# Optimization experiments

Measured on AMD Instinct MI355X. Metric: run time of the kernel, lower is better.

## Reference

```python
import jax, jax.numpy as jnp
import numpy as np
import math

B, S, D_MODEL, HEADS, HK = 1024, 81, 64, 4, 16  # S=81 from dim1=5184/64; HK=head dim
FFN, LAYERS, NCLS = 128, 2, 16
EPS = 1e-5


def setup_inputs() -> dict:
    key = jax.random.key(0)
    ks = iter(jax.random.split(key, 40))
    def rn(shape, scale=1.0):
        return jax.random.normal(next(ks), shape, jnp.float32) * scale
    d = {}
    d['X'] = rn((B, 1, 30, 13, 13))
    d['c3w'] = rn((8, 1, 3, 3, 3), 0.1); d['c3b'] = jnp.zeros((8,), jnp.float32)
    d['bn3g'] = jnp.ones((8,), jnp.float32); d['bn3b'] = jnp.zeros((8,), jnp.float32)
    d['c2w'] = rn((64, 224, 3, 3), 0.05); d['c2b'] = jnp.zeros((64,), jnp.float32)
    d['bn2g'] = jnp.ones((64,), jnp.float32); d['bn2b'] = jnp.zeros((64,), jnp.float32)
    d['wq'] = rn((LAYERS, HEADS, D_MODEL, HK), 1.0 / D_MODEL)
    d['wk'] = rn((LAYERS, HEADS, D_MODEL, HK), 1.0 / D_MODEL)
    d['wv'] = rn((LAYERS, HEADS, D_MODEL, HK), 1.0 / D_MODEL)
    d['wg'] = rn((LAYERS, D_MODEL, D_MODEL), 1.0 / D_MODEL)
    d['wo'] = rn((LAYERS, D_MODEL, D_MODEL), 1.0 / D_MODEL)
    d['gng'] = jnp.ones((LAYERS, D_MODEL), jnp.float32); d['gnb'] = jnp.zeros((LAYERS, D_MODEL), jnp.float32)
    d['ln1g'] = jnp.ones((LAYERS, D_MODEL), jnp.float32); d['ln1b'] = jnp.zeros((LAYERS, D_MODEL), jnp.float32)
    d['ln2g'] = jnp.ones((LAYERS, D_MODEL), jnp.float32); d['ln2b'] = jnp.zeros((LAYERS, D_MODEL), jnp.float32)
    d['fw1'] = rn((LAYERS, D_MODEL, FFN), 0.05); d['fb1'] = jnp.zeros((LAYERS, FFN), jnp.float32)
    d['fw2'] = rn((LAYERS, FFN, D_MODEL), 0.05); d['fb2'] = jnp.zeros((LAYERS, D_MODEL), jnp.float32)
    d['nn1w'] = rn((S * D_MODEL, NCLS), 0.02); d['nn1b'] = rn((NCLS,), 1e-6)
    return d


def _bn(x, g, b, axes):
    # BatchNorm in training mode (module default): batch statistics, biased var
    mu = x.mean(axes, keepdims=True)
    var = x.var(axes, keepdims=True)
    shp = [1] * x.ndim; shp[1] = -1
    return (x - mu) / jnp.sqrt(var + EPS) * g.reshape(shp) + b.reshape(shp)


def _ln(x, g, b):
    mu = x.mean(-1, keepdims=True)
    var = x.var(-1, keepdims=True)
    return (x - mu) / jnp.sqrt(var + EPS) * g + b


def _rot2(x):
    # rotate_every_two: (x0,x1,x2,x3,...) -> (-x1,x0,-x3,x2,...)
    x1, x2 = x[..., ::2], x[..., 1::2]
    return jnp.stack((-x2, x1), axis=-1).reshape(x.shape)


def _xpos_tables():
    scale = (jnp.arange(0, HK, 2, dtype=jnp.float32) + 0.4 * HK) / (1.4 * HK)  # (HK/2,)
    pos = jnp.arange(S, dtype=jnp.float32)
    xs = scale[None, :] ** (pos[:, None] / 512.0)                               # (S, HK/2)
    inv_freq = 1.0 / (10000.0 ** (jnp.arange(HK // 2, dtype=jnp.float32) / (HK // 2)))
    ang = pos[:, None] * inv_freq[None, :]
    sin, cos = jnp.sin(ang), jnp.cos(ang)
    dup = lambda m: jnp.repeat(m, 2, axis=-1)                                   # (S, HK)
    return dup(cos * xs), dup(sin * xs), dup(cos / xs), dup(sin / xs)


def _decay_mask():
    g = 1.0 - jnp.exp(jnp.linspace(math.log(1 / 32), math.log(1 / 512), HEADS))
    nm = jnp.arange(S)[:, None] - jnp.arange(S)[None, :]
    return jnp.where(nm >= 0, g[:, None, None] ** nm, 0.0)                      # (H,S,S)


def _forward(X, c3w, c3b, bn3g, bn3b, c2w, c2b, bn2g, bn2b,
             wq, wk, wv, wg, wo, gng, gnb, ln1g, ln1b, ln2g, ln2b,
             fw1, fb1, fw2, fb2, nn1w, nn1b):
    # Convnet front-end
    x = jax.lax.conv_general_dilated(X, c3w, (1, 1, 1), 'VALID',
                                     dimension_numbers=('NCDHW', 'OIDHW', 'NCDHW'))
    x = x + c3b[None, :, None, None, None]
    x = jax.nn.relu(_bn(x, bn3g, bn3b, (0, 2, 3, 4)))        # (B,8,28,11,11)
    x = x.reshape(B, 8 * 28, 11, 11)                           # 'b c h w y -> b (c h) w y'
    x = jax.lax.conv_general_dilated(x, c2w, (1, 1), 'VALID',
                                     dimension_numbers=('NCHW', 'OIHW', 'NCHW'))
    x = x + c2b[None, :, None, None]
    x = jax.nn.relu(_bn(x, bn2g, bn2b, (0, 2, 3)))           # (B,64,9,9)
    x = x.transpose(0, 2, 3, 1).reshape(B, S, D_MODEL)        # 'b c h w -> b (h w) c'

    cu, su, cd, sd = _xpos_tables()
    Dm = _decay_mask()
    for l in range(LAYERS):
        h = _ln(x, ln1g[l], ln1b[l])
        # per-head retention (parallel form)
        Q = jnp.einsum('bsd,hdk->bhsk', h, wq[l])
        K = jnp.einsum('bsd,hdk->bhsk', h, wk[l])
        V = jnp.einsum('bsd,hdk->bhsk', h, wv[l])
        Q = Q * cu + _rot2(Q) * su                            # xpos upscale
        K = K * cd + _rot2(K) * sd                            # xpos downscale
        att = jnp.einsum('bhsk,bhtk->bhst', Q, K) * Dm[None]  # decay-masked scores
        Yh = jnp.einsum('bhst,bhtv->bhsv', att, V)            # (B,H,S,HK)
        # GroupNorm(heads, v_dim) on (B*S, v_dim): per-(b,s,head) normalization
        mu = Yh.mean(-1, keepdims=True)
        var = Yh.var(-1, keepdims=True)
        Yh = (Yh - mu) / jnp.sqrt(var + EPS)
        Yc = Yh.transpose(0, 2, 1, 3).reshape(B, S, D_MODEL) * gng[l] + gnb[l]
        G = h @ wg[l]
        y = (G * jax.nn.sigmoid(G) * Yc) @ wo[l] + x          # swish gate + residual
        h2 = _ln(y, ln2g[l], ln2b[l])
        x = jax.nn.gelu(h2 @ fw1[l] + fb1[l], approximate=False) @ fw2[l] + fb2[l] + y
    return x.reshape(B, S * D_MODEL) @ nn1w + nn1b            # (B, NCLS)


def reference(X, c3w, c3b, bn3g, bn3b, c2w, c2b, bn2g, bn2b,
              wq, wk, wv, wg, wo, gng, gnb, ln1g, ln1b, ln2g, ln2b,
              fw1, fb1, fw2, fb2, nn1w, nn1b):
    return _forward(X, c3w, c3b, bn3g, bn3b, c2w, c2b, bn2g, bn2b,
                    wq, wk, wv, wg, wo, gng, gnb, ln1g, ln1b, ln2g, ln2b,
                    fw1, fb1, fw2, fb2, nn1w, nn1b)
```

## Files before the change

### kernel.cpp

```cpp
#include <hip/hip_runtime.h>
#include <math.h>

#define EPS 1e-5f

#define OFF_A  0u
#define OFF_X0 0u
#define OFF_Y  31850496u
#define OFF_CP 31850496u
#define OFF_WC 32374784u
#define OFF_B  47775744u
#define OFF_P  53084160u
#define OFF_RT 53084160u
#define OFF_ST 53215232u

#define WB_QKV 0u
#define WB_WG  24576u
#define WB_WO  32768u
#define WB_FW1 40960u
#define WB_FW2 57344u

typedef __attribute__((ext_vector_type(8))) short short8;
typedef __attribute__((ext_vector_type(4))) float f32x4;

__device__ inline unsigned short f2bf(float f) {
  unsigned int x = __float_as_uint(f);
  unsigned int r = x + 0x7fffu + ((x >> 16) & 1u);
  return (unsigned short)(r >> 16);
}
__device__ inline float bf2f(unsigned short h) {
  return __uint_as_float(((unsigned int)h) << 16);
}

__global__ __launch_bounds__(256) void kd1_conv1(const float* X, const float* c3w,
                                                 const float* c3b, float* ws) {
  __shared__ float Xi[5070];
  __shared__ float w3[216];
  int tid = threadIdx.x, b = blockIdx.x;
  for (int u = tid; u < 5070; u += 256) Xi[u] = X[(size_t)b*5070 + u];
  if (tid < 216) w3[tid] = c3w[tid];
  __syncthreads();
  if (tid >= 224) return;
  int o1 = tid / 28, dd = tid - o1*28;
  float wr[27];
#pragma unroll
  for (int k = 0; k < 27; ++k) wr[k] = w3[o1*27 + k];
  float bias = c3b[o1];
  unsigned short* Ao = (unsigned short*)(ws + OFF_A) + (size_t)b*27104;
  float S = 0.f, Q = 0.f;
  for (int h = 0; h < 11; ++h) {
    const float* base = Xi + dd*169 + h*13;
    float c0[9], c1[9], c2[9];
#pragma unroll
    for (int j = 0; j < 9; ++j) {
      int kd = j / 3, kh = j - kd*3;
      const float* rp = base + kd*169 + kh*13;
      c0[j] = rp[0]; c1[j] = rp[1]; c2[j] = rp[2];
    }
#pragma unroll
    for (int w = 0; w < 11; ++w) {
      float a = bias;
#pragma unroll
      for (int j = 0; j < 9; ++j) {
        a = fmaf(c0[j], wr[j*3+0], a);
        a = fmaf(c1[j], wr[j*3+1], a);
        a = fmaf(c2[j], wr[j*3+2], a);
      }
      Ao[(h*11 + w)*224 + tid] = f2bf(a);
      S += a; Q += a*a;
      if (w < 10) {
#pragma unroll
        for (int j = 0; j < 9; ++j) {
          int kd = j / 3, kh = j - kd*3;
          c0[j] = c1[j]; c1[j] = c2[j];
          c2[j] = base[kd*169 + kh*13 + w + 3];
        }
      }
    }
  }
  ws[OFF_CP + b*448 + tid]       = S;
  ws[OFF_CP + b*448 + 224 + tid] = Q;
}

__global__ void kd3_bn1fin(const float* ws_in, float* ws,
                           const float* bn3g, const float* bn3b) {
  __shared__ float sS[256], sQ[256];
  int t = threadIdx.x;
  int o1 = t >> 5, j = t & 31;
  float S = 0.f, Q = 0.f;
  for (int b = j; b < 1024; b += 32) {
    const float* P = ws_in + OFF_CP + b*448 + o1*28;
    for (int dd = 0; dd < 28; ++dd) { S += P[dd]; Q += P[224 + dd]; }
  }
  sS[t] = S; sQ[t] = Q;
  __syncthreads();
  if (j == 0) {
    float Ss = 0.f, Qs = 0.f;
    for (int k = 0; k < 32; ++k) { Ss += sS[o1*32 + k]; Qs += sQ[o1*32 + k]; }
    float n = 3469312.f;
    float mean = Ss / n;
    float var = Qs / n - mean*mean;
    float sc = bn3g[o1] * rsqrtf(var + EPS);
    ws[OFF_ST + o1]     = sc;
    ws[OFF_ST + 8 + o1] = bn3b[o1] - mean*sc;
  }
}

__global__ void k0wc(const float* c2w, float* ws) {
  int i = blockIdx.x*256 + threadIdx.x;
  if (i >= 129024) return;
  int ci = i % 224; int r = i / 224; int kpos = r % 9; int oc = r / 9;
  ((unsigned short*)(ws + OFF_WC))[i] = f2bf(c2w[oc*2016 + ci*9 + kpos]);
}

__global__ __launch_bounds__(256) void kd5_conv2_mfma(const float* ws_in, const float* c2b,
                                                      float* ws) {
  __shared__ unsigned short InT[121*232];
  __shared__ float bn1s[224], bn1sh[224];
  const int tid  = threadIdx.x;
  const int b    = blockIdx.x;
  const int wid  = tid >> 6;
  const int lane = tid & 63;
  const int lane15 = lane & 15;
  const int kgrp   = lane >> 4;
  if (tid < 224) {
    int o1 = tid / 28;
    bn1s[tid]  = ws_in[OFF_ST + o1];
    bn1sh[tid] = ws_in[OFF_ST + 8 + o1];
  }
  __syncthreads();
  const unsigned short* Ab = (const unsigned short*)(ws_in + OFF_A) + (size_t)b*27104;
  for (int e = tid; e < 27104; e += 256) {
    int pos = e / 224, ci = e - pos*224;
    float v = fmaxf(bn1s[ci]*bf2f(Ab[e]) + bn1sh[ci], 0.f);
    InT[pos*232 + ci] = f2bf(v);
  }
  __syncthreads();

  int r0[6];
#pragma unroll
  for (int mt = 0; mt < 6; ++mt) {
    int s = mt*16 + lane15; if (s > 80) s = 80;
    int y = s / 9;
    r0[mt] = y*11 + (s - y*9);
  }
  const unsigned short* wcb = (const unsigned short*)(ws_in + OFF_WC);
  const int col = wid*16 + lane15;
  f32x4 acc[6];
#pragma unroll
  for (int mt = 0; mt < 6; ++mt) acc[mt] = (f32x4){0.f,0.f,0.f,0.f};

  for (int kpos = 0; kpos < 9; ++kpos) {
    int ki = kpos / 3, kj = kpos - ki*3;
    int roff = ki*11 + kj;
    const unsigned short* wcp = wcb + ((size_t)col*9 + kpos)*224 + kgrp*8;
#pragma unroll
    for (int Ks = 0; Ks < 7; ++Ks) {
      short8 bf = *(const short8*)(wcp + Ks*32);
#pragma unroll
      for (int mt = 0; mt < 6; ++mt) {
        short8 af = *(const short8*)(InT + (r0[mt] + roff)*232 + Ks*32 + kgrp*8);
        acc[mt] = __builtin_amdgcn_mfma_f32_16x16x32_bf16(af, bf, acc[mt], 0, 0, 0);
      }
    }
  }
  float bias = c2b[col];
  float* Bb = ws + OFF_B + (size_t)b*5184 + col*81;
  float S = 0.f, Q = 0.f;
#pragma unroll
  for (int mt = 0; mt < 6; ++mt) {
#pragma unroll
    for (int r = 0; r < 4; ++r) {
      int s = mt*16 + kgrp*4 + r;
      if (s < 81) {
        float v = acc[mt][r] + bias;
        Bb[s] = v;
        S += v; Q += v*v;
      }
    }
  }
  S += __shfl_xor(S, 16); S += __shfl_xor(S, 32);
  Q += __shfl_xor(Q, 16); Q += __shfl_xor(Q, 32);
  if (kgrp == 0) {
    ws[OFF_P + b*128 + col]      = S;
    ws[OFF_P + b*128 + 64 + col] = Q;
  }
}

__global__ void kd7_bn2fin(float* ws, const float* bn2g, const float* bn2b) {
  int t = threadIdx.x;
  float S = 0.f, Q = 0.f;
  for (int b = 0; b < 1024; ++b) {
    S += ws[OFF_P + b*128 + t];
    Q += ws[OFF_P + b*128 + 64 + t];
  }
  float n = 82944.f;
  float mean = S / n;
  float var = Q / n - mean * mean;
  float sc = bn2g[t] * rsqrtf(var + EPS);
  ws[OFF_ST + 16 + t] = sc;
  ws[OFF_ST + 80 + t] = bn2b[t] - mean * sc;
}

__global__ void k0rot(float* ws) {
  int i = blockIdx.x * 256 + threadIdx.x;
  if (i >= 1296) return;
  int m = i / 648, r = i - m*648;
  int s = r >> 3, pp = r & 7;
  float scale = (2.f*pp + 6.4f) / 22.4f;
  float xs = powf(scale, (float)s / 512.f);
  float invf = powf(10000.f, -(float)pp / 8.f);
  float ang = (float)s * invf;
  float cx = cosf(ang), sn = sinf(ang);
  float cu = m ? cx/xs : cx*xs;
  float su = m ? sn/xs : sn*xs;
  ws[OFF_RT + i*2]     = cu;
  ws[OFF_RT + i*2 + 1] = su;
}

__global__ __launch_bounds__(256) void kd8_tokens(float* ws) {
  int idx = blockIdx.x * 256 + threadIdx.x;
  if (idx >= 5308416) return;
  int o = idx % 64;
  int s = (idx / 64) % 81;
  int b = idx / 5184;
  float v = ws[OFF_ST + 16 + o] * ws[OFF_B + (size_t)b*5184 + o*81 + s] + ws[OFF_ST + 80 + o];
  ws[OFF_X0 + idx] = fmaxf(v, 0.f);
}

__global__ void k0pack(const float* wq, const float* wk, const float* wv,
                       const float* wg, const float* wo, const float* fw1,
                       const float* fw2, float* ws) {
  int i = blockIdx.x * 256 + threadIdx.x;
  unsigned short* wb = (unsigned short*)(ws + OFF_B);
  if (i < 24576) {
    int l = i / 12288, r = i % 12288;
    int p = r / 6144; r %= 6144;
    int col = r / 64, k = r % 64;
    int m = col >> 5, h2 = (col >> 4) & 1, kk = col & 15;
    const float* src = (m==0) ? wq : (m==1) ? wk : wv;
    wb[i] = f2bf(src[((l*4 + 2*p + h2)*64 + k)*16 + kk]);
  } else if (i < 32768) {
    int j = i - 24576;
    int l = j / 4096, col = (j / 64) & 63, k = j & 63;
    wb[i] = f2bf(wg[(l*64 + k)*64 + col]);
  } else if (i < 40960) {
    int j = i - 32768;
    int l = j / 4096, col = (j / 64) & 63, k = j & 63;
    wb[i] = f2bf(wo[(l*64 + k)*64 + col]);
  } else if (i < 57344) {
    int j = i - 40960;
    int l = j / 8192, col = (j / 64) % 128, k = j & 63;
    wb[i] = f2bf(fw1[(l*64 + k)*128 + col]);
  } else if (i < 73728) {
    int j = i - 57344;
    int l = j / 8192, col = (j / 128) & 63, k = j % 128;
    wb[i] = f2bf(fw2[(l*128 + k)*64 + col]);
  }
}

__global__ __launch_bounds__(256) void fa_layer(const float* ws_in, float* ws,
    const float* ln1g, const float* ln1b, const float* gng, const float* gnb, int l)
{
  __shared__ __align__(16) float sm[15018];
  unsigned short* Hb = (unsigned short*)sm;
  float* P0 = sm + 3840;
  float* P1 = sm + 6594;
  float* P2 = sm + 9348;
  float* P3 = sm + 12102;
  float* XT = sm + 3840;
  unsigned short* Zb = (unsigned short*)(sm + 9348);
  float* muv = sm + 14856;
  float* rsd = sm + 14937;
  const int tid  = threadIdx.x;
  const int b    = blockIdx.x;
  const int wid  = tid >> 6;
  const int lane = tid & 63;
  const int lane15 = lane & 15;
  const int kgrp   = lane >> 4;
  const float* xg = ws_in + OFF_X0 + (size_t)b * 5184;
  const float* rtab = ws_in + OFF_RT;
  const unsigned short* wb = (const unsigned short*)(ws_in + OFF_B);

  for (int u = tid; u < 5184; u += 256) XT[u] = xg[u];
  __syncthreads();
  if (tid < 81) {
    const float* xr = XT + tid*64;
    float sv = 0.f;
    for (int d = 0; d < 64; ++d) sv += xr[d];
    float mean = sv * (1.f/64.f);
    float sq = 0.f;
    for (int d = 0; d < 64; ++d) { float dv = xr[d]-mean; sq += dv*dv; }
    muv[tid] = mean;
    rsd[tid] = rsqrtf(sq*(1.f/64.f) + EPS);
  }
  __syncthreads();
  for (int u = tid; u < 5184; u += 256) {
    int s = u >> 6, d = u & 63;
    Hb[s*80 + d] = f2bf((XT[u] - muv[s])*rsd[s]*ln1g[l*64+d] + ln1b[l*64+d]);
  }
  for (int e = tid; e < 1200; e += 256) Hb[81*80 + e] = 0;
  __syncthreads();

  for (int p = 0; p < 2; ++p) {
    float* QB = p ? P1 : P0;
    float* KB = p ? P2 : P1;
    float* VB = p ? P3 : P2;
    const unsigned short* Bb = wb + WB_QKV + (size_t)(l*2 + p)*6144;
#pragma unroll
    for (int t = 0; t < 3; ++t) {
      int task = wid*3 + t;
      int Nt = task >> 1, mh = task & 1;
      f32x4 acc[3];
#pragma unroll
      for (int m3 = 0; m3 < 3; ++m3) acc[m3] = (f32x4){0.f,0.f,0.f,0.f};
#pragma unroll
      for (int Ks = 0; Ks < 2; ++Ks) {
        short8 bf = *(const short8*)(Bb + (size_t)(Nt*16 + lane15)*64 + Ks*32 + kgrp*8);
#pragma unroll
        for (int m3 = 0; m3 < 3; ++m3) {
          int r = (mh*3 + m3)*16 + lane15;
          short8 af = *(const short8*)(Hb + r*80 + Ks*32 + kgrp*8);
          acc[m3] = __builtin_amdgcn_mfma_f32_16x16x32_bf16(af, bf, acc[m3], 0, 0, 0);
        }
      }
      int col = Nt*16 + lane15;
      int m = col >> 5, idx = col & 31;
      float* dst = (m==0) ? QB : (m==1) ? KB : VB;
#pragma unroll
      for (int m3 = 0; m3 < 3; ++m3) {
#pragma unroll
        for (int r4 = 0; r4 < 4; ++r4) {
          int s = (mh*3 + m3)*16 + kgrp*4 + r4;
          if (s < 81) dst[s*34 + idx] = acc[m3][r4];
        }
      }
    }
    __syncthreads();
    for (int u = tid; u < 2592; u += 256) {
      int m = u / 1296;
      int rem = u - m*1296;
      int h2 = rem / 648;
      int r2 = rem - h2*648;
      int pp = r2 & 7, s = r2 >> 3;
      const float* rt = rtab + (m*648 + s*8 + pp)*2;
      float cu = rt[0], su = rt[1];
      float* ptr = (m ? KB : QB) + s*34 + h2*16 + 2*pp;
      float a = ptr[0], bb2 = ptr[1];
      ptr[0] = a*cu - bb2*su;
      ptr[1] = bb2*cu + a*su;
    }
    __syncthreads();
    if (tid < 162) {
      int h2 = tid & 1, s = tid >> 1;
      int hd = 2*p + h2;
      float g = 1.f - expf(-3.4657359f + (float)hd * (-0.92419624f));
      float lg = log2f(g);
      float q[16];
#pragma unroll
      for (int k = 0; k < 16; ++k) q[k] = QB[s*34 + h2*16 + k];
      float yh[16];
#pragma unroll
      for (int v = 0; v < 16; ++v) yh[v] = 0.f;
      for (int tt = 0; tt <= s; ++tt) {
        const float* Kr = KB + tt*34 + h2*16;
        float a = 0.f;
#pragma unroll
        for (int k = 0; k < 16; ++k) a = fmaf(q[k], Kr[k], a);
        a *= exp2f((float)(s - tt) * lg);
        const float* Vr = VB + tt*34 + h2*16;
#pragma unroll
        for (int v = 0; v < 16; ++v) yh[v] = fmaf(a, Vr[v], yh[v]);
      }
      float sv = 0.f;
#pragma unroll
      for (int v = 0; v < 16; ++v) sv += yh[v];
      float mean = sv * (1.f/16.f);
      float sq = 0.f;
#pragma unroll
      for (int v = 0; v < 16; ++v) { float dv = yh[v]-mean; sq += dv*dv; }
      float rstd = rsqrtf(sq*(1.f/16.f) + EPS);
#pragma unroll
      for (int v = 0; v < 16; ++v) {
        int col = hd*16 + v;
        QB[s*34 + h2*16 + v] = (yh[v]-mean)*rstd*gng[l*64+col] + gnb[l*64+col];
      }
    }
    __syncthreads();
  }

  {
    for (int e = tid; e < 1200; e += 256) Zb[81*80 + e] = 0;
    const unsigned short* Gb = wb + WB_WG + (size_t)l*4096;
    f32x4 acc[6];
#pragma unroll
    for (int mt = 0; mt < 6; ++mt) acc[mt] = (f32x4){0.f,0.f,0.f,0.f};
#pragma unroll
    for (int Ks = 0; Ks < 2; ++Ks) {
      short8 bf = *(const short8*)(Gb + (size_t)(wid*16 + lane15)*64 + Ks*32 + kgrp*8);
#pragma unroll
      for (int mt = 0; mt < 6; ++mt) {
        short8 af = *(const short8*)(Hb + (mt*16 + lane15)*80 + Ks*32 + kgrp*8);
        acc[mt] = __builtin_amdgcn_mfma_f32_16x16x32_bf16(af, bf, acc[mt], 0, 0, 0);
      }
    }
    int col = wid*16 + lane15;
    const float* gnb_ = (col < 32) ? P0 : P1;
#pragma unroll
    for (int mt = 0; mt < 6; ++mt) {
#pragma unroll
      for (int r4 = 0; r4 < 4; ++r4) {
        int s = mt*16 + kgrp*4 + r4;
        if (s < 81) {
          float g = acc[mt][r4];
          float sig = 1.f/(1.f+expf(-g));
          Zb[s*80 + col] = f2bf(g*sig*gnb_[s*34 + (col & 31)]);
        }
      }
    }
  }
  __syncthreads();

  {
    const unsigned short* Ob = wb + WB_WO + (size_t)l*4096;
    float* yg = ws + OFF_Y + (size_t)b * 5184;
    f32x4 acc[6];
#pragma unroll
    for (int mt = 0; mt < 6; ++mt) acc[mt] = (f32x4){0.f,0.f,0.f,0.f};
#pragma unroll
    for (int Ks = 0; Ks < 2; ++Ks) {
      short8 bf = *(const short8*)(Ob + (size_t)(wid*16 + lane15)*64 + Ks*32 + kgrp*8);
#pragma unroll
      for (int mt = 0; mt < 6; ++mt) {
        short8 af = *(const short8*)(Zb + (mt*16 + lane15)*80 + Ks*32 + kgrp*8);
        acc[mt] = __builtin_amdgcn_mfma_f32_16x16x32_bf16(af, bf, acc[mt], 0, 0, 0);
      }
    }
    int col = wid*16 + lane15;
#pragma unroll
    for (int mt = 0; mt < 6; ++mt) {
#pragma unroll
      for (int r4 = 0; r4 < 4; ++r4) {
        int s = mt*16 + kgrp*4 + r4;
        if (s < 81) {
          int u = s*64 + col;
          yg[u] = acc[mt][r4] + xg[u];
        }
      }
    }
  }
}

__global__ __launch_bounds__(256) void ff_layer(const float* ws_in, float* ws,
    const float* fb1, const float* fb2, const float* ln2g, const float* ln2b, int l)
{
  __shared__ __align__(16) float sm[10914];
  unsigned short* H2b = (unsigned short*)sm;
  unsigned short* F1b = (unsigned short*)(sm + 3840);
  float* XT = sm + 3840;
  float* muv = sm + 10752;
  float* rsd = sm + 10833;
  const int tid  = threadIdx.x;
  const int b    = blockIdx.x;
  const int wid  = tid >> 6;
  const int lane = tid & 63;
  const int lane15 = lane & 15;
  const int kgrp   = lane >> 4;
  const float* yg = ws_in + OFF_Y + (size_t)b * 5184;
  const unsigned short* wb = (const unsigned short*)(ws_in + OFF_B);

  for (int u = tid; u < 5184; u += 256) XT[u] = yg[u];
  __syncthreads();
  if (tid < 81) {
    const float* xr = XT + tid*64;
    float sv = 0.f;
    for (int d = 0; d < 64; ++d) sv += xr[d];
    float mean = sv * (1.f/64.f);
    float sq = 0.f;
    for (int d = 0; d < 64; ++d) { float dv = xr[d]-mean; sq += dv*dv; }
    muv[tid] = mean;
    rsd[tid] = rsqrtf(sq*(1.f/64.f) + EPS);
  }
  __syncthreads();
  for (int u = tid; u < 5184; u += 256) {
    int s = u >> 6, d = u & 63;
    H2b[s*80 + d] = f2bf((XT[u] - muv[s])*rsd[s]*ln2g[l*64+d] + ln2b[l*64+d]);
  }
  for (int e = tid; e < 1200; e += 256) H2b[81*80 + e] = 0;
  __syncthreads();

  {
    for (int e = tid; e < 2160; e += 256) F1b[81*144 + e] = 0;
    const unsigned short* Wb1 = wb + WB_FW1 + (size_t)l*8192;
#pragma unroll
    for (int t = 0; t < 4; ++t) {
      int task = wid*4 + t;
      int Nt = task >> 1, mh = task & 1;
      f32x4 acc[3];
#pragma unroll
      for (int m3 = 0; m3 < 3; ++m3) acc[m3] = (f32x4){0.f,0.f,0.f,0.f};
#pragma unroll
      for (int Ks = 0; Ks < 2; ++Ks) {
        short8 bf = *(const short8*)(Wb1 + (size_t)(Nt*16 + lane15)*64 + Ks*32 + kgrp*8);
#pragma unroll
        for (int m3 = 0; m3 < 3; ++m3) {
          int r = (mh*3 + m3)*16 + lane15;
          short8 af = *(const short8*)(H2b + r*80 + Ks*32 + kgrp*8);
          acc[m3] = __builtin_amdgcn_mfma_f32_16x16x32_bf16(af, bf, acc[m3], 0, 0, 0);
        }
      }
      int col = Nt*16 + lane15;
#pragma unroll
      for (int m3 = 0; m3 < 3; ++m3) {
#pragma unroll
        for (int r4 = 0; r4 < 4; ++r4) {
          int s = (mh*3 + m3)*16 + kgrp*4 + r4;
          if (s < 81) {
            float pp = acc[m3][r4] + fb1[l*128 + col];
            F1b[s*144 + col] = f2bf(0.5f*pp*(1.f + erff(pp*0.70710678118f)));
          }
        }
      }
    }
  }
  __syncthreads();

  {
    const unsigned short* Wb2 = wb + WB_FW2 + (size_t)l*8192;
    float* xg = ws + OFF_X0 + (size_t)b * 5184;
    f32x4 acc[6];
#pragma unroll
    for (int mt = 0; mt < 6; ++mt) acc[mt] = (f32x4){0.f,0.f,0.f,0.f};
#pragma unroll
    for (int Ks = 0; Ks < 4; ++Ks) {
      short8 bf = *(const short8*)(Wb2 + (size_t)(wid*16 + lane15)*128 + Ks*32 + kgrp*8);
#pragma unroll
      for (int mt = 0; mt < 6; ++mt) {
        short8 af = *(const short8*)(F1b + (mt*16 + lane15)*144 + Ks*32 + kgrp*8);
        acc[mt] = __builtin_amdgcn_mfma_f32_16x16x32_bf16(af, bf, acc[mt], 0, 0, 0);
      }
    }
    int col = wid*16 + lane15;
#pragma unroll
    for (int mt = 0; mt < 6; ++mt) {
#pragma unroll
      for (int r4 = 0; r4 < 4; ++r4) {
        int s = mt*16 + kgrp*4 + r4;
        if (s < 81) {
          int u = s*64 + col;
          xg[u] = acc[mt][r4] + fb2[l*64 + col] + yg[u];
        }
      }
    }
  }
}

__global__ __launch_bounds__(256) void fcls(const float* ws_in, const float* nn1w,
                                            const float* nn1b, float* out) {
  __shared__ float red[256];
  const int tid = threadIdx.x;
  const int b = blockIdx.x;
  const float* Xr = ws_in + OFF_X0 + (size_t)b * 5184;
  int c = tid & 15, chunk = tid >> 4;
  int i0 = chunk * 324;
  float a = 0.f;
  for (int i = 0; i < 324; ++i)
    a = fmaf(Xr[i0+i], nn1w[(size_t)(i0+i)*16 + c], a);
  red[tid] = a;
  __syncthreads();
  if (tid < 16) {
    float s = nn1b[tid];
#pragma unroll
    for (int j = 0; j < 16; ++j) s += red[j*16 + tid];
    out[b*16 + tid] = s;
  }
}

extern "C" void kernel_launch(void* const* d_in, const int* in_sizes, int n_in,
                              void* d_out, int out_size, void* d_ws, size_t ws_size,
                              hipStream_t stream) {
  const float* X    = (const float*)d_in[0];
  const float* c3w  = (const float*)d_in[1];
  const float* c3b  = (const float*)d_in[2];
  const float* bn3g = (const float*)d_in[3];
  const float* bn3b = (const float*)d_in[4];
  const float* c2w  = (const float*)d_in[5];
  const float* c2b  = (const float*)d_in[6];
  const float* bn2g = (const float*)d_in[7];
  const float* bn2b = (const float*)d_in[8];
  const float* wq   = (const float*)d_in[9];
  const float* wk   = (const float*)d_in[10];
  const float* wv   = (const float*)d_in[11];
  const float* wg   = (const float*)d_in[12];
  const float* wo   = (const float*)d_in[13];
  const float* gng  = (const float*)d_in[14];
  const float* gnb  = (const float*)d_in[15];
  const float* ln1g = (const float*)d_in[16];
  const float* ln1b = (const float*)d_in[17];
  const float* ln2g = (const float*)d_in[18];
  const float* ln2b = (const float*)d_in[19];
  const float* fw1  = (const float*)d_in[20];
  const float* fb1  = (const float*)d_in[21];
  const float* fw2  = (const float*)d_in[22];
  const float* fb2  = (const float*)d_in[23];
  const float* nn1w = (const float*)d_in[24];
  const float* nn1b = (const float*)d_in[25];
  float* ws = (float*)d_ws;
  float* out = (float*)d_out;

  k0wc<<<504, 256, 0, stream>>>(c2w, ws);
  kd1_conv1<<<1024, 256, 0, stream>>>(X, c3w, c3b, ws);
  kd3_bn1fin<<<1, 256, 0, stream>>>(ws, ws, bn3g, bn3b);
  kd5_conv2_mfma<<<1024, 256, 0, stream>>>(ws, c2b, ws);
  kd7_bn2fin<<<1, 64, 0, stream>>>(ws, bn2g, bn2b);
  k0rot<<<6, 256, 0, stream>>>(ws);
  kd8_tokens<<<20736, 256, 0, stream>>>(ws);
  k0pack<<<288, 256, 0, stream>>>(wq, wk, wv, wg, wo, fw1, fw2, ws);

  for (int l = 0; l < 2; ++l) {
    fa_layer<<<1024, 256, 0, stream>>>(ws, ws, ln1g, ln1b, gng, gnb, l);
    ff_layer<<<1024, 256, 0, stream>>>(ws, ws, fb1, fb2, ln2g, ln2b, l);
  }

  fcls<<<1024, 256, 0, stream>>>(ws, nn1w, nn1b, out);
}
```

Measured before the change: 532.8 us.

## Shrink shared memory via bf16 Q/K/V buffers and tighter row padding

Stores the per-head Q, K, V and GroupNorm output scratch in shared memory as bf16 instead of fp32, and cuts the padded row stride of the bf16 MFMA operand tiles from 80 to 72 (and 144 to 136). Both kernels then need less LDS per block, so more blocks can be resident per CU. The cost is extra bf16 conversions in the rotary and attention inner loops and lower precision for Q/K/V and the attention output. The new strides also change the LDS bank-conflict pattern for the 16-byte MFMA operand loads.

```diff
diff --git a/kernel.cpp b/kernel.cpp
--- a/kernel.cpp
+++ b/kernel.cpp
@@ -261,16 +261,16 @@
 __global__ __launch_bounds__(256) void fa_layer(const float* ws_in, float* ws,
     const float* ln1g, const float* ln1b, const float* gng, const float* gnb, int l)
 {
-  __shared__ __align__(16) float sm[15018];
-  unsigned short* Hb = (unsigned short*)sm;
-  float* P0 = sm + 3840;
-  float* P1 = sm + 6594;
-  float* P2 = sm + 9348;
-  float* P3 = sm + 12102;
-  float* XT = sm + 3840;
-  unsigned short* Zb = (unsigned short*)(sm + 9348);
-  float* muv = sm + 14856;
-  float* rsd = sm + 14937;
+  __shared__ __align__(16) float sm[9834];
+  unsigned short* Hb  = (unsigned short*)sm;
+  unsigned short* P0u = (unsigned short*)(sm + 3456);
+  unsigned short* P1u = (unsigned short*)(sm + 4833);
+  unsigned short* P2u = (unsigned short*)(sm + 6210);
+  unsigned short* P3u = (unsigned short*)(sm + 7587);
+  unsigned short* Zb  = (unsigned short*)(sm + 6216);
+  float* XT  = sm + 3456;
+  float* muv = sm + 9672;
+  float* rsd = sm + 9753;
   const int tid  = threadIdx.x;
   const int b    = blockIdx.x;
   const int wid  = tid >> 6;
@@ -296,15 +296,15 @@
   __syncthreads();
   for (int u = tid; u < 5184; u += 256) {
     int s = u >> 6, d = u & 63;
-    Hb[s*80 + d] = f2bf((XT[u] - muv[s])*rsd[s]*ln1g[l*64+d] + ln1b[l*64+d]);
-  }
-  for (int e = tid; e < 1200; e += 256) Hb[81*80 + e] = 0;
+    Hb[s*72 + d] = f2bf((XT[u] - muv[s])*rsd[s]*ln1g[l*64+d] + ln1b[l*64+d]);
+  }
+  for (int e = tid; e < 1080; e += 256) Hb[81*72 + e] = 0;
   __syncthreads();
 
   for (int p = 0; p < 2; ++p) {
-    float* QB = p ? P1 : P0;
-    float* KB = p ? P2 : P1;
-    float* VB = p ? P3 : P2;
+    unsigned short* QB = p ? P1u : P0u;
+    unsigned short* KB = p ? P2u : P1u;
+    unsigned short* VB = p ? P3u : P2u;
     const unsigned short* Bb = wb + WB_QKV + (size_t)(l*2 + p)*6144;
 #pragma unroll
     for (int t = 0; t < 3; ++t) {
@@ -319,19 +319,19 @@
 #pragma unroll
         for (int m3 = 0; m3 < 3; ++m3) {
           int r = (mh*3 + m3)*16 + lane15;
-          short8 af = *(const short8*)(Hb + r*80 + Ks*32 + kgrp*8);
+          short8 af = *(const short8*)(Hb + r*72 + Ks*32 + kgrp*8);
           acc[m3] = __builtin_amdgcn_mfma_f32_16x16x32_bf16(af, bf, acc[m3], 0, 0, 0);
         }
       }
       int col = Nt*16 + lane15;
       int m = col >> 5, idx = col & 31;
-      float* dst = (m==0) ? QB : (m==1) ? KB : VB;
+      unsigned short* dst = (m==0) ? QB : (m==1) ? KB : VB;
 #pragma unroll
       for (int m3 = 0; m3 < 3; ++m3) {
 #pragma unroll
         for (int r4 = 0; r4 < 4; ++r4) {
           int s = (mh*3 + m3)*16 + kgrp*4 + r4;
-          if (s < 81) dst[s*34 + idx] = acc[m3][r4];
+          if (s < 81) dst[s*34 + idx] = f2bf(acc[m3][r4]);
         }
       }
     }
@@ -344,10 +344,10 @@
       int pp = r2 & 7, s = r2 >> 3;
       const float* rt = rtab + (m*648 + s*8 + pp)*2;
       float cu = rt[0], su = rt[1];
-      float* ptr = (m ? KB : QB) + s*34 + h2*16 + 2*pp;
-      float a = ptr[0], bb2 = ptr[1];
-      ptr[0] = a*cu - bb2*su;
-      ptr[1] = bb2*cu + a*su;
+      unsigned short* ptr = (m ? KB : QB) + s*34 + h2*16 + 2*pp;
+      float a = bf2f(ptr[0]), bb2 = bf2f(ptr[1]);
+      ptr[0] = f2bf(a*cu - bb2*su);
+      ptr[1] = f2bf(bb2*cu + a*su);
     }
     __syncthreads();
     if (tid < 162) {
@@ -357,19 +357,19 @@
       float lg = log2f(g);
       float q[16];
 #pragma unroll
-      for (int k = 0; k < 16; ++k) q[k] = QB[s*34 + h2*16 + k];
+      for (int k = 0; k < 16; ++k) q[k] = bf2f(QB[s*34 + h2*16 + k]);
       float yh[16];
 #pragma unroll
       for (int v = 0; v < 16; ++v) yh[v] = 0.f;
       for (int tt = 0; tt <= s; ++tt) {
-        const float* Kr = KB + tt*34 + h2*16;
+        const unsigned short* Kr = KB + tt*34 + h2*16;
         float a = 0.f;
 #pragma unroll
-        for (int k = 0; k < 16; ++k) a = fmaf(q[k], Kr[k], a);
+        for (int k = 0; k < 16; ++k) a = fmaf(q[k], bf2f(Kr[k]), a);
         a *= exp2f((float)(s - tt) * lg);
-        const float* Vr = VB + tt*34 + h2*16;
-#pragma unroll
-        for (int v = 0; v < 16; ++v) yh[v] = fmaf(a, Vr[v], yh[v]);
+        const unsigned short* Vr = VB + tt*34 + h2*16;
+#pragma unroll
+        for (int v = 0; v < 16; ++v) yh[v] = fmaf(a, bf2f(Vr[v]), yh[v]);
       }
       float sv = 0.f;
 #pragma unroll
@@ -382,14 +382,14 @@
 #pragma unroll
       for (int v = 0; v < 16; ++v) {
         int col = hd*16 + v;
-        QB[s*34 + h2*16 + v] = (yh[v]-mean)*rstd*gng[l*64+col] + gnb[l*64+col];
+        QB[s*34 + h2*16 + v] = f2bf((yh[v]-mean)*rstd*gng[l*64+col] + gnb[l*64+col]);
       }
     }
     __syncthreads();
   }
 
   {
-    for (int e = tid; e < 1200; e += 256) Zb[81*80 + e] = 0;
+    for (int e = tid; e < 1080; e += 256) Zb[81*72 + e] = 0;
     const unsigned short* Gb = wb + WB_WG + (size_t)l*4096;
     f32x4 acc[6];
 #pragma unroll
@@ -399,12 +399,12 @@
       short8 bf = *(const short8*)(Gb + (size_t)(wid*16 + lane15)*64 + Ks*32 + kgrp*8);
 #pragma unroll
       for (int mt = 0; mt < 6; ++mt) {
-        short8 af = *(const short8*)(Hb + (mt*16 + lane15)*80 + Ks*32 + kgrp*8);
+        short8 af = *(const short8*)(Hb + (mt*16 + lane15)*72 + Ks*32 + kgrp*8);
         acc[mt] = __builtin_amdgcn_mfma_f32_16x16x32_bf16(af, bf, acc[mt], 0, 0, 0);
       }
     }
     int col = wid*16 + lane15;
-    const float* gnb_ = (col < 32) ? P0 : P1;
+    const unsigned short* gnb_ = (col < 32) ? P0u : P1u;
 #pragma unroll
     for (int mt = 0; mt < 6; ++mt) {
 #pragma unroll
@@ -413,7 +413,7 @@
         if (s < 81) {
           float g = acc[mt][r4];
           float sig = 1.f/(1.f+expf(-g));
-          Zb[s*80 + col] = f2bf(g*sig*gnb_[s*34 + (col & 31)]);
+          Zb[s*72 + col] = f2bf(g*sig*bf2f(gnb_[s*34 + (col & 31)]));
         }
       }
     }
@@ -431,7 +431,7 @@
       short8 bf = *(const short8*)(Ob + (size_t)(wid*16 + lane15)*64 + Ks*32 + kgrp*8);
 #pragma unroll
       for (int mt = 0; mt < 6; ++mt) {
-        short8 af = *(const short8*)(Zb + (mt*16 + lane15)*80 + Ks*32 + kgrp*8);
+        short8 af = *(const short8*)(Zb + (mt*16 + lane15)*72 + Ks*32 + kgrp*8);
         acc[mt] = __builtin_amdgcn_mfma_f32_16x16x32_bf16(af, bf, acc[mt], 0, 0, 0);
       }
     }
@@ -453,12 +453,12 @@
 __global__ __launch_bounds__(256) void ff_layer(const float* ws_in, float* ws,
     const float* fb1, const float* fb2, const float* ln2g, const float* ln2b, int l)
 {
-  __shared__ __align__(16) float sm[10914];
+  __shared__ __align__(16) float sm[10146];
   unsigned short* H2b = (unsigned short*)sm;
-  unsigned short* F1b = (unsigned short*)(sm + 3840);
-  float* XT = sm + 3840;
-  float* muv = sm + 10752;
-  float* rsd = sm + 10833;
+  unsigned short* F1b = (unsigned short*)(sm + 3456);
+  float* XT = sm + 3456;
+  float* muv = sm + 9984;
+  float* rsd = sm + 10065;
   const int tid  = threadIdx.x;
   const int b    = blockIdx.x;
   const int wid  = tid >> 6;
@@ -483,13 +483,13 @@
   __syncthreads();
   for (int u = tid; u < 5184; u += 256) {
     int s = u >> 6, d = u & 63;
-    H2b[s*80 + d] = f2bf((XT[u] - muv[s])*rsd[s]*ln2g[l*64+d] + ln2b[l*64+d]);
-  }
-  for (int e = tid; e < 1200; e += 256) H2b[81*80 + e] = 0;
+    H2b[s*72 + d] = f2bf((XT[u] - muv[s])*rsd[s]*ln2g[l*64+d] + ln2b[l*64+d]);
+  }
+  for (int e = tid; e < 1080; e += 256) H2b[81*72 + e] = 0;
   __syncthreads();
 
   {
-    for (int e = tid; e < 2160; e += 256) F1b[81*144 + e] = 0;
+    for (int e = tid; e < 2040; e += 256) F1b[81*136 + e] = 0;
     const unsigned short* Wb1 = wb + WB_FW1 + (size_t)l*8192;
 #pragma unroll
     for (int t = 0; t < 4; ++t) {
@@ -504,7 +504,7 @@
 #pragma unroll
         for (int m3 = 0; m3 < 3; ++m3) {
           int r = (mh*3 + m3)*16 + lane15;
-          short8 af = *(const short8*)(H2b + r*80 + Ks*32 + kgrp*8);
+          short8 af = *(const short8*)(H2b + r*72 + Ks*32 + kgrp*8);
           acc[m3] = __builtin_amdgcn_mfma_f32_16x16x32_bf16(af, bf, acc[m3], 0, 0, 0);
         }
       }
@@ -516,7 +516,7 @@
           int s = (mh*3 + m3)*16 + kgrp*4 + r4;
           if (s < 81) {
             float pp = acc[m3][r4] + fb1[l*128 + col];
-            F1b[s*144 + col] = f2bf(0.5f*pp*(1.f + erff(pp*0.70710678118f)));
+            F1b[s*136 + col] = f2bf(0.5f*pp*(1.f + erff(pp*0.70710678118f)));
           }
         }
       }
@@ -535,7 +535,7 @@
       short8 bf = *(const short8*)(Wb2 + (size_t)(wid*16 + lane15)*128 + Ks*32 + kgrp*8);
 #pragma unroll
       for (int mt = 0; mt < 6; ++mt) {
-        short8 af = *(const short8*)(F1b + (mt*16 + lane15)*144 + Ks*32 + kgrp*8);
+        short8 af = *(const short8*)(F1b + (mt*16 + lane15)*136 + Ks*32 + kgrp*8);
         acc[mt] = __builtin_amdgcn_mfma_f32_16x16x32_bf16(af, bf, acc[mt], 0, 0, 0);
       }
     }
```

After: 614.9 us. 15.4% more time.
